# Kernel tuning notes

Measured on AMD Instinct MI355X. Metric: run time of the kernel, lower is better.

The kernel has to match this reference:

```python
import jax, jax.numpy as jnp
import numpy as np

N, D, DOUT = 10000, 128, 128
KS, KN, KC, NCENTER, HID = 32, 16, 16, 3, 32  # HID = D // 4


def setup_inputs() -> dict:
    key = jax.random.key(0)
    ks = jax.random.split(key, 32)
    p = lambda i, shape: jax.random.normal(ks[i], shape, dtype=jnp.float32) * 0.05
    return {
        "ids": jnp.arange(N, dtype=jnp.int64) if jax.config.jax_enable_x64 else jnp.arange(N, dtype=jnp.int32),
        "feats": jax.random.normal(ks[0], (N, D), dtype=jnp.float32),
        "cluster_idx": jax.random.randint(ks[1], (N, NCENTER, KC), 0, N),
        "struct_idx": jax.random.randint(ks[2], (N, KS), 0, N),
        "epo": 100,
        # VertexConv (cluster): Transform convKK grouped conv -> (k,k,D) weight, (k,k) bias; convK1 -> (k,) weight, scalar bias
        "wKK_c": p(3, (KC, KC, D)), "bKK_c": p(4, (KC, KC)), "wK1_c": p(5, (KC,)), "bK1_c": p(6, ()),
        # VertexConv (knn)
        "wKK_n": p(7, (KN, KN, D)), "bKK_n": p(8, (KN, KN)), "wK1_n": p(9, (KN,)), "bK1_n": p(10, ()),
        # VertexConv (structure)
        "wKK_s": p(11, (KS, KS, D)), "bKK_s": p(12, (KS, KS)), "wK1_s": p(13, (KS,)), "bK1_s": p(14, ()),
        # EdgeConv attention MLP: Linear(D, D//4) -> ReLU -> Linear(D//4, 1)
        "ec_w1": p(15, (D, HID)), "ec_b1": p(16, (HID,)), "ec_w2": p(17, (HID,)), "ec_b2": p(18, ()),
        # Final Linear(D, DOUT)
        "fc_w": p(19, (D, DOUT)), "fc_b": p(20, (DOUT,)),
    }


def vertex_conv(x, wKK, bKK, wK1, bK1):
    # x: (N, k, d). Grouped Conv1d(k, k*k, d, groups=k): mult[n,i,j] = <wKK[i,j], x[n,i]> + bKK[i,j]
    mult = jnp.einsum("nid,ijd->nij", x, wKK) + bKK
    mult = jax.nn.softmax(mult, axis=-1)                 # softmax over last dim
    transformed = jnp.einsum("nij,njd->nid", mult, x)    # (N, k, d)
    # Conv1d(k, 1, 1): weighted sum over the k channels
    return jnp.einsum("nkd,k->nd", transformed, wK1) + bK1


def reference(ids, feats, cluster_idx, struct_idx, epo,
              wKK_c, bKK_c, wK1_c, bK1_c,
              wKK_n, bKK_n, wK1_n, bK1_n,
              wKK_s, bKK_s, wK1_s, bK1_s,
              ec_w1, ec_b1, ec_w2, ec_b2, fc_w, fc_b):
    # epo=100 >= all warmups -> all three hyperedge branches active (static).
    # --- cluster hyperedges (precomputed kmeans index table) ---
    c_feats = feats[cluster_idx[ids]]                    # (N, n_center, kc, d)
    hyperedge = [vertex_conv(c_feats[:, c], wKK_c, bKK_c, wK1_c, bK1_c)
                 for c in range(NCENTER)]
    # --- knn hyperedge: cosine similarity + topk (cos_dis) ---
    nrm = jnp.maximum(jnp.linalg.norm(feats, axis=1, keepdims=True), 1e-12)
    xn = feats / nrm
    sim = xn @ xn.T                                      # (N, N) -- memory-dominant
    _, knn_idx = jax.lax.top_k(sim, KN)                  # (N, kn)
    hyperedge.append(vertex_conv(feats[knn_idx[ids]], wKK_n, bKK_n, wK1_n, bK1_n))
    # --- structure hyperedge (precomputed sampled edge_dict table) ---
    hyperedge.append(vertex_conv(feats[struct_idx[ids]], wKK_s, bKK_s, wK1_s, bK1_s))
    x = jnp.stack(hyperedge, axis=1)                     # (N, t, d), t = n_center + 2
    # EdgeConv: MLP attention over the t hyperedges, softmax along t, weighted sum
    h = jax.nn.relu(jnp.einsum("ntd,dh->nth", x, ec_w1) + ec_b1)
    scores = jax.nn.softmax(jnp.einsum("nth,h->nt", h, ec_w2) + ec_b2, axis=1)
    agg = jnp.einsum("nt,ntd->nd", scores, x)            # (N, d)
    # final fc + relu (dropout = identity in eval)
    return jax.nn.relu(agg @ fc_w + fc_b)
```

## Files before the change

### kernel.cpp

```cpp
#include <hip/hip_runtime.h>
#include <cmath>


#define N_NODES 10000
#define D 128
#define DQ 32
#define NCB 3
#define T_HE 5
#define HID_SZ 32
#define NCH 16
#define CHUNK 625
#define TOPK 16
#define TOPM 32

typedef __attribute__((ext_vector_type(8))) short short8;
typedef __attribute__((ext_vector_type(8))) _Float16 half8;
typedef __attribute__((ext_vector_type(4))) float f32x4;
typedef __attribute__((ext_vector_type(16))) float f32x16;

__device__ __forceinline__ unsigned bf16rne(float f) {
  unsigned u = __float_as_uint(f);
  return (u + 0x7FFFu + ((u >> 16) & 1u)) >> 16;
}

__global__ __launch_bounds__(256) void kpre(const float* __restrict__ feats,
                                            const float* __restrict__ wc,
                                            const float* __restrict__ wn,
                                            const float* __restrict__ wstr,
                                            unsigned short* __restrict__ xnh,
                                            _Float16* __restrict__ fH16,
                                            double* __restrict__ normD,
                                            _Float16* __restrict__ wH16) {
  int bx = blockIdx.x;
  int tid = threadIdx.x;
  if (bx < 2500) {
    int n = bx * 4 + (tid >> 6);
    int lane = tid & 63;
    float2 v = ((const float2*)(feats + (size_t)n * D))[lane];
    _Float16 p2[2] = {(_Float16)v.x, (_Float16)v.y};
    ((unsigned*)(fH16 + (size_t)n * D))[lane] = *(const unsigned*)p2;
    double ss = (double)v.x * (double)v.x + (double)v.y * (double)v.y;
#pragma unroll
    for (int o = 32; o > 0; o >>= 1) ss += __shfl_xor(ss, o);
    double nd = fmax(sqrt(ss), 1e-12);
    if (lane == 0) normD[n] = nd;
    float inv = (float)(1.0 / nd);
    ((unsigned*)(xnh + (size_t)n * D))[lane] = bf16rne(v.x * inv) | (bf16rne(v.y * inv) << 16);
  } else {
    int p = (bx - 2500) * 256 + tid;
    if (p >= 98304) return;
    int e = p * 2;
    float2 v;
    if (e < 32768) v = *(const float2*)(wc + e);
    else if (e < 65536) v = *(const float2*)(wn + (e - 32768));
    else v = *(const float2*)(wstr + (e - 65536));
    _Float16 p2[2] = {(_Float16)v.x, (_Float16)v.y};
    ((unsigned*)wH16)[p] = *(const unsigned*)p2;
  }
}

__device__ __forceinline__ void ceu(unsigned& a, unsigned& b) {
  unsigned lo = min(a, b), hi = max(a, b);
  a = lo; b = hi;
}
__device__ __forceinline__ void ceu64(unsigned long long& a, unsigned long long& b) {
  unsigned long long lo = min(a, b), hi = max(a, b);
  a = lo; b = hi;
}
__device__ __forceinline__ void sort16_asc(unsigned (&v)[16]) {
#pragma unroll
  for (int k = 2; k <= 16; k <<= 1) {
#pragma unroll
    for (int j = k >> 1; j > 0; j >>= 1) {
#pragma unroll
      for (int i = 0; i < 16; i++) {
        int x = i ^ j;
        if (x > i) {
          if ((i & k) == 0) ceu(v[i], v[x]);
          else ceu(v[x], v[i]);
        }
      }
    }
  }
}
__device__ __forceinline__ void merge16_asc(unsigned (&run)[16], const unsigned (&b)[16]) {
  unsigned m[16];
#pragma unroll
  for (int i = 0; i < 16; i++) m[i] = max(run[i], b[15 - i]);
#pragma unroll
  for (int j = 8; j > 0; j >>= 1) {
#pragma unroll
    for (int i = 0; i < 16; i++) {
      if ((i & j) == 0) ceu(m[i], m[i + j]);
    }
  }
#pragma unroll
  for (int i = 0; i < 16; i++) run[i] = m[i];
}

__global__ __launch_bounds__(256, 4) void ksim(const unsigned short* __restrict__ xnh,
                                               unsigned* __restrict__ cand) {
  __shared__ short Bb[16 * 128 * 8];
  int tid = threadIdx.x;
  int w = tid >> 6, lane = tid & 63, l31 = lane & 31, lh = lane >> 5;
  int row0 = blockIdx.x * 128 + w * 32;
  int chunk = blockIdx.y;
  int cbase = chunk * CHUNK;

  short8 afr[8];
  {
    int ar = min(row0 + l31, N_NODES - 1);
    const short8* ap = (const short8*)(xnh + (size_t)ar * D);
#pragma unroll
    for (int ks = 0; ks < 8; ks++) afr[ks] = ap[ks * 2 + lh];
  }

  unsigned run[16];
#pragma unroll
  for (int s = 0; s < 16; s++) run[s] = 0u;

  for (int ti = 0; ti < 5; ti++) {
    int tb = cbase + ti * 128;
    __syncthreads();
    {
      int ci = tid >> 1, h = tid & 1;
      int gcol = min(tb + ci, N_NODES - 1);
      const short8* gp = (const short8*)(xnh + (size_t)gcol * D);
      short8* bp = (short8*)Bb;
#pragma unroll
      for (int i = 0; i < 8; i++) bp[(h * 8 + i) * 128 + ci] = gp[h * 8 + i];
    }
    __syncthreads();

    const short8* bv = (const short8*)Bb;
#pragma unroll
    for (int half = 0; half < 2; half++) {
      f32x16 acc[2];
#pragma unroll
      for (int nj = 0; nj < 2; nj++)
#pragma unroll
        for (int r = 0; r < 16; r++) acc[nj][r] = 0.f;
#pragma unroll
      for (int ks = 0; ks < 8; ks++) {
        int kp = ks * 2 + lh;
#pragma unroll
        for (int nj = 0; nj < 2; nj++) {
          int ni = half * 2 + nj;
          short8 af = bv[kp * 128 + ni * 32 + l31];
          acc[nj] = __builtin_amdgcn_mfma_f32_32x32x16_bf16(af, afr[ks], acc[nj], 0, 0, 0);
        }
      }
#pragma unroll
      for (int nj = 0; nj < 2; nj++) {
        int ni = half * 2 + nj;
        unsigned bt[16];
#pragma unroll
        for (int reg = 0; reg < 16; reg++) {
          int m = (reg & 3) + 8 * (reg >> 2) + 4 * lh;
          int cic = ti * 128 + ni * 32 + m;
          unsigned bb = __float_as_uint(acc[nj][reg]);
          unsigned mu = (bb & 0x80000000u) ? ~bb : (bb | 0x80000000u);
          bt[reg] = (cic < CHUNK) ? ((mu & 0xFFFFFC00u) | (unsigned)(1023 - cic)) : 0u;
        }
        sort16_asc(bt);
        merge16_asc(run, bt);
      }
    }
  }
  {
    unsigned other[16];
#pragma unroll
    for (int s = 0; s < 16; s++) other[s] = (unsigned)__shfl_xor((int)run[s], 32);
    merge16_asc(run, other);
  }
  int grow = row0 + l31;
  if (lh == 0 && grow < N_NODES) {
    unsigned* o = cand + ((size_t)grow * NCH + chunk) * 16;
#pragma unroll
    for (int i = 0; i < 16; i += 4)
      *(uint4*)(o + i) = make_uint4(run[i], run[i + 1], run[i + 2], run[i + 3]);
  }
}

__global__ __launch_bounds__(64) void kmerge(const unsigned* __restrict__ cand,
                                             int* __restrict__ candIdx) {
  int row = blockIdx.x * 64 + threadIdx.x;
  if (row >= N_NODES) return;
  unsigned long long run[TOPM];
#pragma unroll
  for (int s = 0; s < TOPM; s++) run[s] = 0ull;
  const uint4* c4 = (const uint4*)(cand + (size_t)row * (NCH * 16));
  for (int ch = 0; ch < NCH; ch++) {
    unsigned b[16];
#pragma unroll
    for (int q = 0; q < 4; q++) {
      uint4 t = c4[ch * 4 + q];
      b[q * 4 + 0] = t.x; b[q * 4 + 1] = t.y;
      b[q * 4 + 2] = t.z; b[q * 4 + 3] = t.w;
    }
    unsigned base = (unsigned)(ch * CHUNK);
    unsigned long long b64[16];
#pragma unroll
    for (int s = 0; s < 16; s++) {
      unsigned k = b[s];
      unsigned gcol = base + (1023u - (k & 1023u));
      b64[s] = ((unsigned long long)(k >> 10) << 32) | (unsigned long long)(~gcol);
    }
#pragma unroll
    for (int i = 0; i < 16; i++) run[i] = max(run[i], b64[15 - i]);
#pragma unroll
    for (int j = 16; j > 0; j >>= 1)
#pragma unroll
      for (int i = 0; i < TOPM; i++)
        if ((i & j) == 0) ceu64(run[i], run[i + j]);
  }
  int4* o4 = (int4*)(candIdx + (size_t)row * TOPM);
#pragma unroll
  for (int s = 0; s < TOPM; s += 4) {
    int4 o;
    o.x = (int)(~(unsigned)(run[s + 0] & 0xFFFFFFFFull));
    o.y = (int)(~(unsigned)(run[s + 1] & 0xFFFFFFFFull));
    o.z = (int)(~(unsigned)(run[s + 2] & 0xFFFFFFFFull));
    o.w = (int)(~(unsigned)(run[s + 3] & 0xFFFFFFFFull));
    o4[s >> 2] = o;
  }
}

__global__ __launch_bounds__(256) void krerank(const float* __restrict__ feats,
                                               const double* __restrict__ normD,
                                               const int* __restrict__ candIdx,
                                               int* __restrict__ knn) {
  __shared__ float rowF[D];
  __shared__ double simL[TOPM];
  __shared__ int idxL[TOPM];
  int row = blockIdx.x;
  int tid = threadIdx.x;
  if (tid < DQ)
    ((float4*)rowF)[tid] = ((const float4*)(feats + (size_t)row * D))[tid];
  int c = tid >> 3, part = tid & 7;
  int cnd = candIdx[(size_t)row * TOPM + c];
  __syncthreads();
  const float4* f4 = (const float4*)(feats + (size_t)cnd * D);
  double acc = 0.0;
#pragma unroll
  for (int g = 0; g < 4; g++) {
    float4 v = f4[part * 4 + g];
    const float* rf = &rowF[(part * 4 + g) * 4];
    acc = fma((double)v.x, (double)rf[0], acc);
    acc = fma((double)v.y, (double)rf[1], acc);
    acc = fma((double)v.z, (double)rf[2], acc);
    acc = fma((double)v.w, (double)rf[3], acc);
  }
  acc += __shfl_down(acc, 4);
  acc += __shfl_down(acc, 2);
  acc += __shfl_down(acc, 1);
  if (part == 0) {
    simL[c] = acc / (normD[row] * normD[cnd]);
    idxL[c] = cnd;
  }
  __syncthreads();
  if (tid < TOPM) {
    double s = simL[tid];
    int idx = idxL[tid];
    int rank = 0;
#pragma unroll
    for (int o = 0; o < TOPM; o++) {
      double so = simL[o];
      int io = idxL[o];
      rank += (so > s || (so == s && io < idx)) ? 1 : 0;
    }
    if (rank < TOPK) knn[(size_t)row * TOPK + rank] = idx;
  }
}

__global__ __launch_bounds__(256) void kvcall(
    const _Float16* __restrict__ fH16,
    const int* __restrict__ cluster_idx, const int* __restrict__ knn,
    const int* __restrict__ struct_idx,
    const _Float16* __restrict__ wH16,
    const float* __restrict__ bKK_c, const float* __restrict__ bKK_n,
    const float* __restrict__ bKK_s,
    const float* __restrict__ wK1_c, const float* __restrict__ bK1_c,
    const float* __restrict__ wK1_n, const float* __restrict__ bK1_n,
    const float* __restrict__ wK1_s, const float* __restrict__ bK1_s,
    float* __restrict__ hx) {
  __shared__ int idxL[16][33];
  __shared__ float coefP[4][16][33];
  __shared__ float coefS[16][33];
  int tid = threadIdx.x;
  int z = blockIdx.y;
  int n0 = blockIdx.x * 16;
  int w = tid >> 6, lane = tid & 63, l15 = lane & 15, quad = lane >> 4;
  const half8* fH = (const half8*)fH16;

  if (z < 4) {
    const int* idxTab; int istr, ioff, woff;
    const float* bKK; const float* wK1; const float* bK1p;
    if (z < 3) { idxTab = cluster_idx; istr = NCB * 16; ioff = z * 16; woff = 0;     bKK = bKK_c; wK1 = wK1_c; bK1p = bK1_c; }
    else       { idxTab = knn;         istr = 16;       ioff = 0;      woff = 32768; bKK = bKK_n; wK1 = wK1_n; bK1p = bK1_n; }
    {
      int nn = tid >> 4, i = tid & 15;
      idxL[nn][i] = idxTab[(size_t)(n0 + nn) * istr + ioff + i];
    }
    __syncthreads();
    const half8* wHv = (const half8*)(wH16 + woff);
    f32x4 coef = {0.f, 0.f, 0.f, 0.f};
#pragma unroll
    for (int ii = 0; ii < 4; ii++) {
      int i = w * 4 + ii;
      int rowi = idxL[l15][i];
      float bkk = bKK[i * 16 + l15];
      f32x4 acc = {0.f, 0.f, 0.f, 0.f};
#pragma unroll
      for (int kc = 0; kc < 4; kc++) {
        half8 ah = fH[(size_t)rowi * 16 + kc * 4 + quad];
        half8 bh = wHv[((size_t)i * 16 + l15) * 16 + kc * 4 + quad];
        acc = __builtin_amdgcn_mfma_f32_16x16x32_f16(ah, bh, acc, 0, 0, 0);
      }
      float wki = wK1[i];
#pragma unroll
      for (int r = 0; r < 4; r++) {
        float v = acc[r] + bkk;
        float mx = v;
#pragma unroll
        for (int msk = 1; msk < 16; msk <<= 1) mx = fmaxf(mx, __shfl_xor(mx, msk));
        float e = __expf(v - mx);
        float s = e;
#pragma unroll
        for (int msk = 1; msk < 16; msk <<= 1) s += __shfl_xor(s, msk);
        coef[r] += wki * (e / s);
      }
    }
#pragma unroll
    for (int r = 0; r < 4; r++) coefP[w][quad * 4 + r][l15] = coef[r];
    __syncthreads();
    {
      int nn = tid >> 4, j = tid & 15;
      coefS[nn][j] = coefP[0][nn][j] + coefP[1][nn][j] + coefP[2][nn][j] + coefP[3][nn][j];
    }
    __syncthreads();
    {
      int nl = tid >> 4, g = tid & 15;
      float bk1 = bK1p[0];
      float a8[8];
#pragma unroll
      for (int t = 0; t < 8; t++) a8[t] = bk1;
      for (int j = 0; j < 16; j++) {
        float cf = coefS[nl][j];
        int rowj = idxL[nl][j];
        half8 xv = fH[(size_t)rowj * 16 + g];
#pragma unroll
        for (int e = 0; e < 8; e++) a8[e] = fmaf(cf, (float)xv[e], a8[e]);
      }
      int node = n0 + nl;
      float4* o = (float4*)(hx + ((size_t)node * T_HE + z) * D + g * 8);
      o[0] = make_float4(a8[0], a8[1], a8[2], a8[3]);
      o[1] = make_float4(a8[4], a8[5], a8[6], a8[7]);
    }
  } else {
    for (int e = tid; e < 512; e += 256) {
      int nn = e >> 5, i = e & 31;
      idxL[nn][i] = struct_idx[(size_t)(n0 + nn) * 32 + i];
    }
    __syncthreads();
    const half8* wHv = (const half8*)(wH16 + 65536);
    f32x4 coef0 = {0.f, 0.f, 0.f, 0.f};
    f32x4 coef1 = {0.f, 0.f, 0.f, 0.f};
#pragma unroll
    for (int ii = 0; ii < 8; ii++) {
      int i = w * 8 + ii;
      int rowi = idxL[l15][i];
      float bk0 = bKK_s[i * 32 + l15];
      float bk1v = bKK_s[i * 32 + 16 + l15];
      f32x4 a0 = {0.f, 0.f, 0.f, 0.f};
      f32x4 a1 = {0.f, 0.f, 0.f, 0.f};
#pragma unroll
      for (int kc = 0; kc < 4; kc++) {
        half8 ah = fH[(size_t)rowi * 16 + kc * 4 + quad];
        half8 b0 = wHv[((size_t)i * 32 + l15) * 16 + kc * 4 + quad];
        half8 b1 = wHv[((size_t)i * 32 + 16 + l15) * 16 + kc * 4 + quad];
        a0 = __builtin_amdgcn_mfma_f32_16x16x32_f16(ah, b0, a0, 0, 0, 0);
        a1 = __builtin_amdgcn_mfma_f32_16x16x32_f16(ah, b1, a1, 0, 0, 0);
      }
      float wki = wK1_s[i];
#pragma unroll
      for (int r = 0; r < 4; r++) {
        float v0 = a0[r] + bk0, v1 = a1[r] + bk1v;
        float mx = fmaxf(v0, v1);
#pragma unroll
        for (int msk = 1; msk < 16; msk <<= 1) mx = fmaxf(mx, __shfl_xor(mx, msk));
        float e0 = __expf(v0 - mx), e1 = __expf(v1 - mx);
        float s = e0 + e1;
#pragma unroll
        for (int msk = 1; msk < 16; msk <<= 1) s += __shfl_xor(s, msk);
        float inv = wki / s;
        coef0[r] += e0 * inv;
        coef1[r] += e1 * inv;
      }
    }
#pragma unroll
    for (int r = 0; r < 4; r++) {
      coefP[w][quad * 4 + r][l15] = coef0[r];
      coefP[w][quad * 4 + r][l15 + 16] = coef1[r];
    }
    __syncthreads();
    for (int e = tid; e < 512; e += 256) {
      int nn = e >> 5, j = e & 31;
      coefS[nn][j] = coefP[0][nn][j] + coefP[1][nn][j] + coefP[2][nn][j] + coefP[3][nn][j];
    }
    __syncthreads();
    {
      int nl = tid >> 4, g = tid & 15;
      float bk1 = bK1_s[0];
      float a8[8];
#pragma unroll
      for (int t = 0; t < 8; t++) a8[t] = bk1;
      for (int j = 0; j < 32; j++) {
        float cf = coefS[nl][j];
        int rowj = idxL[nl][j];
        half8 xv = fH[(size_t)rowj * 16 + g];
#pragma unroll
        for (int e = 0; e < 8; e++) a8[e] = fmaf(cf, (float)xv[e], a8[e]);
      }
      int node = n0 + nl;
      float4* o = (float4*)(hx + ((size_t)node * T_HE + 4) * D + g * 8);
      o[0] = make_float4(a8[0], a8[1], a8[2], a8[3]);
      o[1] = make_float4(a8[4], a8[5], a8[6], a8[7]);
    }
  }
}

__global__ __launch_bounds__(256) void kfinal(const float* __restrict__ hx,
    const float* __restrict__ w1, const float* __restrict__ b1,
    const float* __restrict__ w2, const float* __restrict__ b2p,
    const float* __restrict__ fcw, const float* __restrict__ fcb,
    float* __restrict__ out) {
  __shared__ float xL[8][T_HE][D];
  __shared__ float hL[8][T_HE][HID_SZ];
  __shared__ float scL[8][T_HE];
  __shared__ float aggL[8][D];
  int tid = threadIdx.x;
  int n0 = blockIdx.x * 8;
  const float4* hx4 = (const float4*)hx;
  for (int q = tid; q < 8 * T_HE * DQ; q += 256) {
    int nn = q / (T_HE * DQ);
    int rem = q - nn * (T_HE * DQ);
    int t = rem / DQ;
    int dq = rem & 31;
    int node = n0 + nn;
    float4 val = make_float4(0.f, 0.f, 0.f, 0.f);
    if (node < N_NODES) val = hx4[((size_t)node * T_HE + t) * DQ + dq];
    *(float4*)&xL[nn][t][dq << 2] = val;
  }
  __syncthreads();
  for (int q = tid; q < 8 * T_HE * HID_SZ; q += 256) {
    int nn = q / (T_HE * HID_SZ);
    int rem = q - nn * (T_HE * HID_SZ);
    int t = rem / HID_SZ;
    int hh = rem & (HID_SZ - 1);
    float acc = b1[hh];
    const float4* xv4 = (const float4*)xL[nn][t];
    for (int dq = 0; dq < 32; dq++) {
      float4 xv = xv4[dq];
      int db = dq * 4;
      acc = fmaf(xv.x, w1[(db + 0) * HID_SZ + hh], acc);
      acc = fmaf(xv.y, w1[(db + 1) * HID_SZ + hh], acc);
      acc = fmaf(xv.z, w1[(db + 2) * HID_SZ + hh], acc);
      acc = fmaf(xv.w, w1[(db + 3) * HID_SZ + hh], acc);
    }
    hL[nn][t][hh] = fmaxf(acc, 0.f);
  }
  __syncthreads();
  if (tid < 8 * T_HE) {
    int nn = tid / T_HE, t = tid % T_HE;
    float acc = b2p[0];
    for (int hh = 0; hh < HID_SZ; hh++) acc = fmaf(hL[nn][t][hh], w2[hh], acc);
    scL[nn][t] = acc;
  }
  __syncthreads();
  if (tid < 8) {
    float mx = -1e30f;
#pragma unroll
    for (int t = 0; t < T_HE; t++) mx = fmaxf(mx, scL[tid][t]);
    float e[T_HE];
    float s = 0.f;
#pragma unroll
    for (int t = 0; t < T_HE; t++) { e[t] = expf(scL[tid][t] - mx); s += e[t]; }
    float inv = 1.f / s;
#pragma unroll
    for (int t = 0; t < T_HE; t++) scL[tid][t] = e[t] * inv;
  }
  __syncthreads();
  {
    int nn = tid >> 5, dq = tid & 31;
    float4 acc = make_float4(0.f, 0.f, 0.f, 0.f);
#pragma unroll
    for (int t = 0; t < T_HE; t++) {
      float sw = scL[nn][t];
      float4 xv = *(const float4*)&xL[nn][t][dq << 2];
      acc.x = fmaf(sw, xv.x, acc.x);
      acc.y = fmaf(sw, xv.y, acc.y);
      acc.z = fmaf(sw, xv.z, acc.z);
      acc.w = fmaf(sw, xv.w, acc.w);
    }
    *(float4*)&aggL[nn][dq << 2] = acc;
  }
  __syncthreads();
  {
    int dout = tid & 127, g = tid >> 7;
    float a0 = fcb[dout], a1 = a0, a2 = a0, a3 = a0;
    for (int dq = 0; dq < 32; dq++) {
      int db = dq * 4;
      float wv0 = fcw[(db + 0) * 128 + dout];
      float wv1 = fcw[(db + 1) * 128 + dout];
      float wv2 = fcw[(db + 2) * 128 + dout];
      float wv3 = fcw[(db + 3) * 128 + dout];
      float4 v0 = *(const float4*)&aggL[g * 4 + 0][db];
      float4 v1 = *(const float4*)&aggL[g * 4 + 1][db];
      float4 v2 = *(const float4*)&aggL[g * 4 + 2][db];
      float4 v3 = *(const float4*)&aggL[g * 4 + 3][db];
      a0 = fmaf(v0.x, wv0, fmaf(v0.y, wv1, fmaf(v0.z, wv2, fmaf(v0.w, wv3, a0))));
      a1 = fmaf(v1.x, wv0, fmaf(v1.y, wv1, fmaf(v1.z, wv2, fmaf(v1.w, wv3, a1))));
      a2 = fmaf(v2.x, wv0, fmaf(v2.y, wv1, fmaf(v2.z, wv2, fmaf(v2.w, wv3, a2))));
      a3 = fmaf(v3.x, wv0, fmaf(v3.y, wv1, fmaf(v3.z, wv2, fmaf(v3.w, wv3, a3))));
    }
    int nb = n0 + g * 4;
    if (nb + 0 < N_NODES) out[(size_t)(nb + 0) * 128 + dout] = fmaxf(a0, 0.f);
    if (nb + 1 < N_NODES) out[(size_t)(nb + 1) * 128 + dout] = fmaxf(a1, 0.f);
    if (nb + 2 < N_NODES) out[(size_t)(nb + 2) * 128 + dout] = fmaxf(a2, 0.f);
    if (nb + 3 < N_NODES) out[(size_t)(nb + 3) * 128 + dout] = fmaxf(a3, 0.f);
  }
}

extern "C" void kernel_launch(void* const* d_in, const int* in_sizes, int n_in,
                              void* d_out, int out_size, void* d_ws, size_t ws_size,
                              hipStream_t stream) {
  (void)in_sizes; (void)n_in; (void)out_size; (void)ws_size;
  const float* feats       = (const float*)d_in[1];
  const int*   cluster_idx = (const int*)d_in[2];
  const int*   struct_idx  = (const int*)d_in[3];
  const float* wKK_c = (const float*)d_in[5];
  const float* bKK_c = (const float*)d_in[6];
  const float* wK1_c = (const float*)d_in[7];
  const float* bK1_c = (const float*)d_in[8];
  const float* wKK_n = (const float*)d_in[9];
  const float* bKK_n = (const float*)d_in[10];
  const float* wK1_n = (const float*)d_in[11];
  const float* bK1_n = (const float*)d_in[12];
  const float* wKK_s = (const float*)d_in[13];
  const float* bKK_s = (const float*)d_in[14];
  const float* wK1_s = (const float*)d_in[15];
  const float* bK1_s = (const float*)d_in[16];
  const float* ec_w1 = (const float*)d_in[17];
  const float* ec_b1 = (const float*)d_in[18];
  const float* ec_w2 = (const float*)d_in[19];
  const float* ec_b2 = (const float*)d_in[20];
  const float* fc_w  = (const float*)d_in[21];
  const float* fc_b  = (const float*)d_in[22];
  float* out = (float*)d_out;

  char* wsb = (char*)d_ws;
  unsigned short* xnh = (unsigned short*)(wsb);
  unsigned* cand = (unsigned*)(wsb + 2560000);
  int* candIdx = (int*)(wsb + 12800000);
  double* normD = (double*)(wsb + 14080000);
  _Float16* fH16 = (_Float16*)(wsb + 14160000);
  _Float16* wH16 = (_Float16*)(wsb + 16720000);
  int* knnIdx = (int*)(wsb + 46080000);
  float* hx = (float*)(wsb + 46720000);

  kpre<<<2884, 256, 0, stream>>>(feats, wKK_c, wKK_n, wKK_s,
                                 xnh, fH16, normD, wH16);
  ksim<<<dim3(79, NCH), 256, 0, stream>>>(xnh, cand);
  kmerge<<<(N_NODES + 63) / 64, 64, 0, stream>>>(cand, candIdx);
  krerank<<<N_NODES, 256, 0, stream>>>(feats, normD, candIdx, knnIdx);

  kvcall<<<dim3(625, 5), 256, 0, stream>>>(fH16, cluster_idx, knnIdx, struct_idx,
                                           wH16, bKK_c, bKK_n, bKK_s,
                                           wK1_c, bK1_c, wK1_n, bK1_n, wK1_s, bK1_s, hx);

  kfinal<<<1250, 256, 0, stream>>>(hx, ec_w1, ec_b1, ec_w2, ec_b2, fc_w, fc_b, out);
}
```

Before: 375.7 us.

## Fuse KNN-independent vertex convs into similarity kernel to overlap work

```diff
diff --git a/kernel.cpp b/kernel.cpp
--- a/kernel.cpp
+++ b/kernel.cpp
@@ -98,88 +98,277 @@
   for (int i = 0; i < 16; i++) run[i] = m[i];
 }
 
-__global__ __launch_bounds__(256, 4) void ksim(const unsigned short* __restrict__ xnh,
-                                               unsigned* __restrict__ cand) {
-  __shared__ short Bb[16 * 128 * 8];
+__device__ __forceinline__ void vc16_body(int tid, int n0, int tslot,
+    int* idxLm, float* coefPm, float* coefSm,
+    const _Float16* __restrict__ fH16, const _Float16* __restrict__ wH16,
+    const int* __restrict__ idxTab, int istr, int ioff, int woff,
+    const float* __restrict__ bKK, const float* __restrict__ wK1,
+    const float* __restrict__ bK1p, float* __restrict__ hx) {
+  int w = tid >> 6, lane = tid & 63, l15 = lane & 15, quad = lane >> 4;
+  const half8* fH = (const half8*)fH16;
+  {
+    int nn = tid >> 4, i = tid & 15;
+    idxLm[nn * 33 + i] = idxTab[(size_t)(n0 + nn) * istr + ioff + i];
+  }
+  __syncthreads();
+  const half8* wHv = (const half8*)(wH16 + woff);
+  f32x4 coef = {0.f, 0.f, 0.f, 0.f};
+#pragma unroll
+  for (int ii = 0; ii < 4; ii++) {
+    int i = w * 4 + ii;
+    int rowi = idxLm[l15 * 33 + i];
+    float bkk = bKK[i * 16 + l15];
+    f32x4 acc = {0.f, 0.f, 0.f, 0.f};
+#pragma unroll
+    for (int kc = 0; kc < 4; kc++) {
+      half8 ah = fH[(size_t)rowi * 16 + kc * 4 + quad];
+      half8 bh = wHv[((size_t)i * 16 + l15) * 16 + kc * 4 + quad];
+      acc = __builtin_amdgcn_mfma_f32_16x16x32_f16(ah, bh, acc, 0, 0, 0);
+    }
+    float wki = wK1[i];
+#pragma unroll
+    for (int r = 0; r < 4; r++) {
+      float v = acc[r] + bkk;
+      float mx = v;
+#pragma unroll
+      for (int msk = 1; msk < 16; msk <<= 1) mx = fmaxf(mx, __shfl_xor(mx, msk));
+      float e = __expf(v - mx);
+      float s = e;
+#pragma unroll
+      for (int msk = 1; msk < 16; msk <<= 1) s += __shfl_xor(s, msk);
+      coef[r] += wki * (e / s);
+    }
+  }
+#pragma unroll
+  for (int r = 0; r < 4; r++) coefPm[(w * 16 + quad * 4 + r) * 33 + l15] = coef[r];
+  __syncthreads();
+  {
+    int nn = tid >> 4, j = tid & 15;
+    coefSm[nn * 33 + j] = coefPm[(nn) * 33 + j] + coefPm[(16 + nn) * 33 + j] +
+                          coefPm[(32 + nn) * 33 + j] + coefPm[(48 + nn) * 33 + j];
+  }
+  __syncthreads();
+  {
+    int nl = tid >> 4, g = tid & 15;
+    float bk1 = bK1p[0];
+    float a8[8];
+#pragma unroll
+    for (int t = 0; t < 8; t++) a8[t] = bk1;
+    for (int j = 0; j < 16; j++) {
+      float cf = coefSm[nl * 33 + j];
+      int rowj = idxLm[nl * 33 + j];
+      half8 xv = fH[(size_t)rowj * 16 + g];
+#pragma unroll
+      for (int e = 0; e < 8; e++) a8[e] = fmaf(cf, (float)xv[e], a8[e]);
+    }
+    int node = n0 + nl;
+    float4* o = (float4*)(hx + ((size_t)node * T_HE + tslot) * D + g * 8);
+    o[0] = make_float4(a8[0], a8[1], a8[2], a8[3]);
+    o[1] = make_float4(a8[4], a8[5], a8[6], a8[7]);
+  }
+}
+
+__device__ __forceinline__ void vc32_body(int tid, int n0,
+    int* idxLm, float* coefPm, float* coefSm,
+    const _Float16* __restrict__ fH16, const _Float16* __restrict__ wH16,
+    const int* __restrict__ struct_idx,
+    const float* __restrict__ bKK_s, const float* __restrict__ wK1_s,
+    const float* __restrict__ bK1_s, float* __restrict__ hx) {
+  int w = tid >> 6, lane = tid & 63, l15 = lane & 15, quad = lane >> 4;
+  const half8* fH = (const half8*)fH16;
+  for (int e = tid; e < 512; e += 256) {
+    int nn = e >> 5, i = e & 31;
+    idxLm[nn * 33 + i] = struct_idx[(size_t)(n0 + nn) * 32 + i];
+  }
+  __syncthreads();
+  const half8* wHv = (const half8*)(wH16 + 65536);
+  f32x4 coef0 = {0.f, 0.f, 0.f, 0.f};
+  f32x4 coef1 = {0.f, 0.f, 0.f, 0.f};
+#pragma unroll
+  for (int ii = 0; ii < 8; ii++) {
+    int i = w * 8 + ii;
+    int rowi = idxLm[l15 * 33 + i];
+    float bk0 = bKK_s[i * 32 + l15];
+    float bk1v = bKK_s[i * 32 + 16 + l15];
+    f32x4 a0 = {0.f, 0.f, 0.f, 0.f};
+    f32x4 a1 = {0.f, 0.f, 0.f, 0.f};
+#pragma unroll
+    for (int kc = 0; kc < 4; kc++) {
+      half8 ah = fH[(size_t)rowi * 16 + kc * 4 + quad];
+      half8 b0 = wHv[((size_t)i * 32 + l15) * 16 + kc * 4 + quad];
+      half8 b1 = wHv[((size_t)i * 32 + 16 + l15) * 16 + kc * 4 + quad];
+      a0 = __builtin_amdgcn_mfma_f32_16x16x32_f16(ah, b0, a0, 0, 0, 0);
+      a1 = __builtin_amdgcn_mfma_f32_16x16x32_f16(ah, b1, a1, 0, 0, 0);
+    }
+    float wki = wK1_s[i];
+#pragma unroll
+    for (int r = 0; r < 4; r++) {
+      float v0 = a0[r] + bk0, v1 = a1[r] + bk1v;
+      float mx = fmaxf(v0, v1);
+#pragma unroll
+      for (int msk = 1; msk < 16; msk <<= 1) mx = fmaxf(mx, __shfl_xor(mx, msk));
+      float e0 = __expf(v0 - mx), e1 = __expf(v1 - mx);
+      float s = e0 + e1;
+#pragma unroll
+      for (int msk = 1; msk < 16; msk <<= 1) s += __shfl_xor(s, msk);
+      float inv = wki / s;
+      coef0[r] += e0 * inv;
+      coef1[r] += e1 * inv;
+    }
+  }
+#pragma unroll
+  for (int r = 0; r < 4; r++) {
+    coefPm[(w * 16 + quad * 4 + r) * 33 + l15] = coef0[r];
+    coefPm[(w * 16 + quad * 4 + r) * 33 + l15 + 16] = coef1[r];
+  }
+  __syncthreads();
+  for (int e = tid; e < 512; e += 256) {
+    int nn = e >> 5, j = e & 31;
+    coefSm[nn * 33 + j] = coefPm[nn * 33 + j] + coefPm[(16 + nn) * 33 + j] +
+                          coefPm[(32 + nn) * 33 + j] + coefPm[(48 + nn) * 33 + j];
+  }
+  __syncthreads();
+  {
+    int nl = tid >> 4, g = tid & 15;
+    float bk1 = bK1_s[0];
+    float a8[8];
+#pragma unroll
+    for (int t = 0; t < 8; t++) a8[t] = bk1;
+    for (int j = 0; j < 32; j++) {
+      float cf = coefSm[nl * 33 + j];
+      int rowj = idxLm[nl * 33 + j];
+      half8 xv = fH[(size_t)rowj * 16 + g];
+#pragma unroll
+      for (int e = 0; e < 8; e++) a8[e] = fmaf(cf, (float)xv[e], a8[e]);
+    }
+    int node = n0 + nl;
+    float4* o = (float4*)(hx + ((size_t)node * T_HE + 4) * D + g * 8);
+    o[0] = make_float4(a8[0], a8[1], a8[2], a8[3]);
+    o[1] = make_float4(a8[4], a8[5], a8[6], a8[7]);
+  }
+}
+
+__global__ __launch_bounds__(256, 4) void ksimvc(
+    const unsigned short* __restrict__ xnh, unsigned* __restrict__ cand,
+    const _Float16* __restrict__ fH16, const _Float16* __restrict__ wH16,
+    const int* __restrict__ cluster_idx, const int* __restrict__ struct_idx,
+    const float* __restrict__ bKK_c, const float* __restrict__ bKK_s,
+    const float* __restrict__ wK1_c, const float* __restrict__ bK1_c,
+    const float* __restrict__ wK1_s, const float* __restrict__ bK1_s,
+    float* __restrict__ hx) {
+  __shared__ __align__(16) unsigned char smem[32768];
+  int bx = blockIdx.x;
   int tid = threadIdx.x;
-  int w = tid >> 6, lane = tid & 63, l31 = lane & 31, lh = lane >> 5;
-  int row0 = blockIdx.x * 128 + w * 32;
-  int chunk = blockIdx.y;
-  int cbase = chunk * CHUNK;
-
-  short8 afr[8];
-  {
-    int ar = min(row0 + l31, N_NODES - 1);
-    const short8* ap = (const short8*)(xnh + (size_t)ar * D);
-#pragma unroll
-    for (int ks = 0; ks < 8; ks++) afr[ks] = ap[ks * 2 + lh];
-  }
-
-  unsigned run[16];
-#pragma unroll
-  for (int s = 0; s < 16; s++) run[s] = 0u;
-
-  for (int ti = 0; ti < 5; ti++) {
-    int tb = cbase + ti * 128;
-    __syncthreads();
+  int r3 = bx % 3, q3 = bx / 3;
+  if (r3 == 0) {
+    short* Bb = (short*)smem;
+    int rb = q3 % 79, chunk = q3 / 79;
+    int w = tid >> 6, lane = tid & 63, l31 = lane & 31, lh = lane >> 5;
+    int row0 = rb * 128 + w * 32;
+    int cbase = chunk * CHUNK;
+
+    short8 afr[8];
     {
-      int ci = tid >> 1, h = tid & 1;
-      int gcol = min(tb + ci, N_NODES - 1);
-      const short8* gp = (const short8*)(xnh + (size_t)gcol * D);
-      short8* bp = (short8*)Bb;
-#pragma unroll
-      for (int i = 0; i < 8; i++) bp[(h * 8 + i) * 128 + ci] = gp[h * 8 + i];
-    }
-    __syncthreads();
-
-    const short8* bv = (const short8*)Bb;
-#pragma unroll
-    for (int half = 0; half < 2; half++) {
-      f32x16 acc[2];
-#pragma unroll
-      for (int nj = 0; nj < 2; nj++)
-#pragma unroll
-        for (int r = 0; r < 16; r++) acc[nj][r] = 0.f;
-#pragma unroll
-      for (int ks = 0; ks < 8; ks++) {
-        int kp = ks * 2 + lh;
+      int ar = min(row0 + l31, N_NODES - 1);
+      const short8* ap = (const short8*)(xnh + (size_t)ar * D);
+#pragma unroll
+      for (int ks = 0; ks < 8; ks++) afr[ks] = ap[ks * 2 + lh];
+    }
+
+    unsigned run[16];
+#pragma unroll
+    for (int s = 0; s < 16; s++) run[s] = 0u;
+
+    for (int ti = 0; ti < 5; ti++) {
+      int tb = cbase + ti * 128;
+      __syncthreads();
+      {
+        int ci = tid >> 1, h = tid & 1;
+        int gcol = min(tb + ci, N_NODES - 1);
+        const short8* gp = (const short8*)(xnh + (size_t)gcol * D);
+        short8* bp = (short8*)Bb;
+#pragma unroll
+        for (int i = 0; i < 8; i++) bp[(h * 8 + i) * 128 + ci] = gp[h * 8 + i];
+      }
+      __syncthreads();
+
+      const short8* bv = (const short8*)Bb;
+#pragma unroll
+      for (int half = 0; half < 2; half++) {
+        f32x16 acc[2];
+#pragma unroll
+        for (int nj = 0; nj < 2; nj++)
+#pragma unroll
+          for (int r = 0; r < 16; r++) acc[nj][r] = 0.f;
+#pragma unroll
+        for (int ks = 0; ks < 8; ks++) {
+          int kp = ks * 2 + lh;
+#pragma unroll
+          for (int nj = 0; nj < 2; nj++) {
+            int ni = half * 2 + nj;
+            short8 af = bv[kp * 128 + ni * 32 + l31];
+            acc[nj] = __builtin_amdgcn_mfma_f32_32x32x16_bf16(af, afr[ks], acc[nj], 0, 0, 0);
+          }
+        }
 #pragma unroll
         for (int nj = 0; nj < 2; nj++) {
           int ni = half * 2 + nj;
-          short8 af = bv[kp * 128 + ni * 32 + l31];
-          acc[nj] = __builtin_amdgcn_mfma_f32_32x32x16_bf16(af, afr[ks], acc[nj], 0, 0, 0);
+          unsigned bt[16];
+#pragma unroll
+          for (int reg = 0; reg < 16; reg++) {
+            int m = (reg & 3) + 8 * (reg >> 2) + 4 * lh;
+            int cic = ti * 128 + ni * 32 + m;
+            unsigned bb = __float_as_uint(acc[nj][reg]);
+            unsigned mu = (bb & 0x80000000u) ? ~bb : (bb | 0x80000000u);
+            bt[reg] = (cic < CHUNK) ? ((mu & 0xFFFFFC00u) | (unsigned)(1023 - cic)) : 0u;
+          }
+          sort16_asc(bt);
+          merge16_asc(run, bt);
         }
       }
-#pragma unroll
-      for (int nj = 0; nj < 2; nj++) {
-        int ni = half * 2 + nj;
-        unsigned bt[16];
-#pragma unroll
-        for (int reg = 0; reg < 16; reg++) {
-          int m = (reg & 3) + 8 * (reg >> 2) + 4 * lh;
-          int cic = ti * 128 + ni * 32 + m;
-          unsigned bb = __float_as_uint(acc[nj][reg]);
-          unsigned mu = (bb & 0x80000000u) ? ~bb : (bb | 0x80000000u);
-          bt[reg] = (cic < CHUNK) ? ((mu & 0xFFFFFC00u) | (unsigned)(1023 - cic)) : 0u;
-        }
-        sort16_asc(bt);
-        merge16_asc(run, bt);
-      }
-    }
-  }
-  {
-    unsigned other[16];
-#pragma unroll
-    for (int s = 0; s < 16; s++) other[s] = (unsigned)__shfl_xor((int)run[s], 32);
-    merge16_asc(run, other);
-  }
-  int grow = row0 + l31;
-  if (lh == 0 && grow < N_NODES) {
-    unsigned* o = cand + ((size_t)grow * NCH + chunk) * 16;
-#pragma unroll
-    for (int i = 0; i < 16; i += 4)
-      *(uint4*)(o + i) = make_uint4(run[i], run[i + 1], run[i + 2], run[i + 3]);
-  }
+    }
+    {
+      unsigned other[16];
+#pragma unroll
+      for (int s = 0; s < 16; s++) other[s] = (unsigned)__shfl_xor((int)run[s], 32);
+      merge16_asc(run, other);
+    }
+    int grow = row0 + l31;
+    if (lh == 0 && grow < N_NODES) {
+      unsigned* o = cand + ((size_t)grow * NCH + chunk) * 16;
+#pragma unroll
+      for (int i = 0; i < 16; i += 4)
+        *(uint4*)(o + i) = make_uint4(run[i], run[i + 1], run[i + 2], run[i + 3]);
+    }
+  } else {
+    int vid = q3 * 2 + (r3 - 1);
+    if (vid >= 2500) return;
+    int zz = vid / 625, bi = vid - zz * 625;
+    int n0 = bi * 16;
+    int* idxLm = (int*)smem;
+    float* coefPm = (float*)(smem + 2112);
+    float* coefSm = (float*)(smem + 10560);
+    if (zz < 3) {
+      vc16_body(tid, n0, zz, idxLm, coefPm, coefSm, fH16, wH16,
+                cluster_idx, NCB * 16, zz * 16, 0, bKK_c, wK1_c, bK1_c, hx);
+    } else {
+      vc32_body(tid, n0, idxLm, coefPm, coefSm, fH16, wH16,
+                struct_idx, bKK_s, wK1_s, bK1_s, hx);
+    }
+  }
+}
+
+__global__ __launch_bounds__(256, 4) void kvc3(
+    const _Float16* __restrict__ fH16, const _Float16* __restrict__ wH16,
+    const int* __restrict__ knn,
+    const float* __restrict__ bKK_n, const float* __restrict__ wK1_n,
+    const float* __restrict__ bK1_n, float* __restrict__ hx) {
+  __shared__ __align__(16) unsigned char smem[12672];
+  int* idxLm = (int*)smem;
+  float* coefPm = (float*)(smem + 2112);
+  float* coefSm = (float*)(smem + 10560);
+  vc16_body(threadIdx.x, blockIdx.x * 16, 3, idxLm, coefPm, coefSm, fH16, wH16,
+            knn, 16, 0, 32768, bKK_n, wK1_n, bK1_n, hx);
 }
 
 __global__ __launch_bounds__(64) void kmerge(const unsigned* __restrict__ cand,
@@ -270,163 +459,6 @@
       rank += (so > s || (so == s && io < idx)) ? 1 : 0;
     }
     if (rank < TOPK) knn[(size_t)row * TOPK + rank] = idx;
-  }
-}
-
-__global__ __launch_bounds__(256) void kvcall(
-    const _Float16* __restrict__ fH16,
-    const int* __restrict__ cluster_idx, const int* __restrict__ knn,
-    const int* __restrict__ struct_idx,
-    const _Float16* __restrict__ wH16,
-    const float* __restrict__ bKK_c, const float* __restrict__ bKK_n,
-    const float* __restrict__ bKK_s,
-    const float* __restrict__ wK1_c, const float* __restrict__ bK1_c,
-    const float* __restrict__ wK1_n, const float* __restrict__ bK1_n,
-    const float* __restrict__ wK1_s, const float* __restrict__ bK1_s,
-    float* __restrict__ hx) {
-  __shared__ int idxL[16][33];
-  __shared__ float coefP[4][16][33];
-  __shared__ float coefS[16][33];
-  int tid = threadIdx.x;
-  int z = blockIdx.y;
-  int n0 = blockIdx.x * 16;
-  int w = tid >> 6, lane = tid & 63, l15 = lane & 15, quad = lane >> 4;
-  const half8* fH = (const half8*)fH16;
-
-  if (z < 4) {
-    const int* idxTab; int istr, ioff, woff;
-    const float* bKK; const float* wK1; const float* bK1p;
-    if (z < 3) { idxTab = cluster_idx; istr = NCB * 16; ioff = z * 16; woff = 0;     bKK = bKK_c; wK1 = wK1_c; bK1p = bK1_c; }
-    else       { idxTab = knn;         istr = 16;       ioff = 0;      woff = 32768; bKK = bKK_n; wK1 = wK1_n; bK1p = bK1_n; }
-    {
-      int nn = tid >> 4, i = tid & 15;
-      idxL[nn][i] = idxTab[(size_t)(n0 + nn) * istr + ioff + i];
-    }
-    __syncthreads();
-    const half8* wHv = (const half8*)(wH16 + woff);
-    f32x4 coef = {0.f, 0.f, 0.f, 0.f};
-#pragma unroll
-    for (int ii = 0; ii < 4; ii++) {
-      int i = w * 4 + ii;
-      int rowi = idxL[l15][i];
-      float bkk = bKK[i * 16 + l15];
-      f32x4 acc = {0.f, 0.f, 0.f, 0.f};
-#pragma unroll
-      for (int kc = 0; kc < 4; kc++) {
-        half8 ah = fH[(size_t)rowi * 16 + kc * 4 + quad];
-        half8 bh = wHv[((size_t)i * 16 + l15) * 16 + kc * 4 + quad];
-        acc = __builtin_amdgcn_mfma_f32_16x16x32_f16(ah, bh, acc, 0, 0, 0);
-      }
-      float wki = wK1[i];
-#pragma unroll
-      for (int r = 0; r < 4; r++) {
-        float v = acc[r] + bkk;
-        float mx = v;
-#pragma unroll
-        for (int msk = 1; msk < 16; msk <<= 1) mx = fmaxf(mx, __shfl_xor(mx, msk));
-        float e = __expf(v - mx);
-        float s = e;
-#pragma unroll
-        for (int msk = 1; msk < 16; msk <<= 1) s += __shfl_xor(s, msk);
-        coef[r] += wki * (e / s);
-      }
-    }
-#pragma unroll
-    for (int r = 0; r < 4; r++) coefP[w][quad * 4 + r][l15] = coef[r];
-    __syncthreads();
-    {
-      int nn = tid >> 4, j = tid & 15;
-      coefS[nn][j] = coefP[0][nn][j] + coefP[1][nn][j] + coefP[2][nn][j] + coefP[3][nn][j];
-    }
-    __syncthreads();
-    {
-      int nl = tid >> 4, g = tid & 15;
-      float bk1 = bK1p[0];
-      float a8[8];
-#pragma unroll
-      for (int t = 0; t < 8; t++) a8[t] = bk1;
-      for (int j = 0; j < 16; j++) {
-        float cf = coefS[nl][j];
-        int rowj = idxL[nl][j];
-        half8 xv = fH[(size_t)rowj * 16 + g];
-#pragma unroll
-        for (int e = 0; e < 8; e++) a8[e] = fmaf(cf, (float)xv[e], a8[e]);
-      }
-      int node = n0 + nl;
-      float4* o = (float4*)(hx + ((size_t)node * T_HE + z) * D + g * 8);
-      o[0] = make_float4(a8[0], a8[1], a8[2], a8[3]);
-      o[1] = make_float4(a8[4], a8[5], a8[6], a8[7]);
-    }
-  } else {
-    for (int e = tid; e < 512; e += 256) {
-      int nn = e >> 5, i = e & 31;
-      idxL[nn][i] = struct_idx[(size_t)(n0 + nn) * 32 + i];
-    }
-    __syncthreads();
-    const half8* wHv = (const half8*)(wH16 + 65536);
-    f32x4 coef0 = {0.f, 0.f, 0.f, 0.f};
-    f32x4 coef1 = {0.f, 0.f, 0.f, 0.f};
-#pragma unroll
-    for (int ii = 0; ii < 8; ii++) {
-      int i = w * 8 + ii;
-      int rowi = idxL[l15][i];
-      float bk0 = bKK_s[i * 32 + l15];
-      float bk1v = bKK_s[i * 32 + 16 + l15];
-      f32x4 a0 = {0.f, 0.f, 0.f, 0.f};
-      f32x4 a1 = {0.f, 0.f, 0.f, 0.f};
-#pragma unroll
-      for (int kc = 0; kc < 4; kc++) {
-        half8 ah = fH[(size_t)rowi * 16 + kc * 4 + quad];
-        half8 b0 = wHv[((size_t)i * 32 + l15) * 16 + kc * 4 + quad];
-        half8 b1 = wHv[((size_t)i * 32 + 16 + l15) * 16 + kc * 4 + quad];
-        a0 = __builtin_amdgcn_mfma_f32_16x16x32_f16(ah, b0, a0, 0, 0, 0);
-        a1 = __builtin_amdgcn_mfma_f32_16x16x32_f16(ah, b1, a1, 0, 0, 0);
-      }
-      float wki = wK1_s[i];
-#pragma unroll
-      for (int r = 0; r < 4; r++) {
-        float v0 = a0[r] + bk0, v1 = a1[r] + bk1v;
-        float mx = fmaxf(v0, v1);
-#pragma unroll
-        for (int msk = 1; msk < 16; msk <<= 1) mx = fmaxf(mx, __shfl_xor(mx, msk));
-        float e0 = __expf(v0 - mx), e1 = __expf(v1 - mx);
-        float s = e0 + e1;
-#pragma unroll
-        for (int msk = 1; msk < 16; msk <<= 1) s += __shfl_xor(s, msk);
-        float inv = wki / s;
-        coef0[r] += e0 * inv;
-        coef1[r] += e1 * inv;
-      }
-    }
-#pragma unroll
-    for (int r = 0; r < 4; r++) {
-      coefP[w][quad * 4 + r][l15] = coef0[r];
-      coefP[w][quad * 4 + r][l15 + 16] = coef1[r];
-    }
-    __syncthreads();
-    for (int e = tid; e < 512; e += 256) {
-      int nn = e >> 5, j = e & 31;
-      coefS[nn][j] = coefP[0][nn][j] + coefP[1][nn][j] + coefP[2][nn][j] + coefP[3][nn][j];
-    }
-    __syncthreads();
-    {
-      int nl = tid >> 4, g = tid & 15;
-      float bk1 = bK1_s[0];
-      float a8[8];
-#pragma unroll
-      for (int t = 0; t < 8; t++) a8[t] = bk1;
-      for (int j = 0; j < 32; j++) {
-        float cf = coefS[nl][j];
-        int rowj = idxL[nl][j];
-        half8 xv = fH[(size_t)rowj * 16 + g];
-#pragma unroll
-        for (int e = 0; e < 8; e++) a8[e] = fmaf(cf, (float)xv[e], a8[e]);
-      }
-      int node = n0 + nl;
-      float4* o = (float4*)(hx + ((size_t)node * T_HE + 4) * D + g * 8);
-      o[0] = make_float4(a8[0], a8[1], a8[2], a8[3]);
-      o[1] = make_float4(a8[4], a8[5], a8[6], a8[7]);
-    }
   }
 }
 
@@ -571,13 +603,10 @@
 
   kpre<<<2884, 256, 0, stream>>>(feats, wKK_c, wKK_n, wKK_s,
                                  xnh, fH16, normD, wH16);
-  ksim<<<dim3(79, NCH), 256, 0, stream>>>(xnh, cand);
+  ksimvc<<<3792, 256, 0, stream>>>(xnh, cand, fH16, wH16, cluster_idx, struct_idx,
+                                   bKK_c, bKK_s, wK1_c, bK1_c, wK1_s, bK1_s, hx);
   kmerge<<<(N_NODES + 63) / 64, 64, 0, stream>>>(cand, candIdx);
   krerank<<<N_NODES, 256, 0, stream>>>(feats, normD, candIdx, knnIdx);
-
-  kvcall<<<dim3(625, 5), 256, 0, stream>>>(fH16, cluster_idx, knnIdx, struct_idx,
-                                           wH16, bKK_c, bKK_n, bKK_s,
-                                           wK1_c, bK1_c, wK1_n, bK1_n, wK1_s, bK1_s, hx);
-
+  kvc3<<<625, 256, 0, stream>>>(fH16, wH16, knnIdx, bKK_n, wK1_n, bK1_n, hx);
   kfinal<<<1250, 256, 0, stream>>>(hx, ec_w1, ec_b1, ec_w2, ec_b2, fc_w, fc_b, out);
 }
```

Measured after the change: 364.9 us. -2.9%, faster.
